# Optimization experiments

Hardware: AMD Instinct MI355X
Metric: run time of the kernel (lower is better)

Reference implementation:

```python
import jax, jax.numpy as jnp
import numpy as np

EMBED = 1024
MLP = 2048
N_EXPERTS = 8
TOP_K = 2


def setup_inputs() -> dict:
    key = jax.random.key(0)
    ks = jax.random.split(key, 5)
    scale_e = 1.0 / np.sqrt(EMBED)
    scale_m = 1.0 / np.sqrt(MLP)
    x = jax.random.normal(ks[0], (4, 2048, EMBED), dtype=jnp.float32)
    gate_w = jax.random.normal(ks[1], (EMBED, N_EXPERTS), dtype=jnp.float32) * scale_e
    w1 = jax.random.normal(ks[2], (N_EXPERTS, EMBED, MLP), dtype=jnp.float32) * scale_e
    w3 = jax.random.normal(ks[3], (N_EXPERTS, EMBED, MLP), dtype=jnp.float32) * scale_e
    w2 = jax.random.normal(ks[4], (N_EXPERTS, MLP, EMBED), dtype=jnp.float32) * scale_m
    return {"x": x, "gate_w": gate_w, "w1": w1, "w2": w2, "w3": w3}


def reference(x, gate_w, w1, w2, w3):
    B, S, D = x.shape
    xf = x.reshape(-1, D)  # [T, D] tokens
    # Router: softmax over experts, top-k select, renormalize selected weights
    router_logits = xf @ gate_w                      # [T, E]
    routing_weights = jax.nn.softmax(router_logits, axis=-1)
    sel_w, sel_e = jax.lax.top_k(routing_weights, TOP_K)  # [T, K]
    sel_w = sel_w / jnp.sum(sel_w, axis=-1, keepdims=True)
    out = jnp.zeros_like(xf)
    # Loop over the small fixed expert set; tokens not routed to expert e get
    # coefficient 0, matching the gather/scatter-add combine of the original.
    for e in range(N_EXPERTS):
        coef = jnp.sum(jnp.where(sel_e == e, sel_w, 0.0), axis=-1)  # [T]
        h = jax.nn.silu(xf @ w1[e]) * (xf @ w3[e])                  # [T, Mlp] SwiGLU
        out = out + coef[:, None] * (h @ w2[e])                     # [T, D]
    return out.reshape(B, S, D)
```

## Files before the change

kernel.cpp:

```cpp
#include <hip/hip_runtime.h>

#define EMBED 1024
#define MLP   2048
#define MLP2  4096
#define NE    8
#define NTOK  8192
#define RMAX  (2*NTOK + NE*256)

typedef _Float16 f16x8 __attribute__((ext_vector_type(8)));
typedef _Float16 f16x4 __attribute__((ext_vector_type(4)));
typedef float    f32x4 __attribute__((ext_vector_type(4)));

__device__ __forceinline__ void async_copy16(const void* g, void* l) {
  __builtin_amdgcn_global_load_lds(
      (const __attribute__((address_space(1))) unsigned int*)g,
      (__attribute__((address_space(3))) unsigned int*)l, 16, 0, 0);
}

__global__ __launch_bounds__(256) void router_kernel(
    const float* __restrict__ x, const float* __restrict__ gw,
    int* __restrict__ sel_e, float* __restrict__ sel_w, int* __restrict__ counts)
{
  __shared__ float gwt[NE * EMBED];
  __shared__ int cnt[NE];
  int tid = threadIdx.x;
  for (int idx = tid; idx < NE * EMBED; idx += 256) {
    int i = idx >> 3, e = idx & 7;
    gwt[e * EMBED + i] = gw[idx];
  }
  if (tid < NE) cnt[tid] = 0;
  __syncthreads();

  int lane = tid & 63, wv = tid >> 6;
  int t = blockIdx.x * 4 + wv;
  const float4* xr = (const float4*)(x + (size_t)t * EMBED);
  const float4* gt4 = (const float4*)gwt;
  float acc[NE];
  #pragma unroll
  for (int e = 0; e < NE; ++e) acc[e] = 0.f;
  #pragma unroll
  for (int c = 0; c < 4; ++c) {
    float4 xv = xr[c * 64 + lane];
    #pragma unroll
    for (int e = 0; e < NE; ++e) {
      float4 gv = gt4[e * 256 + c * 64 + lane];
      acc[e] += xv.x * gv.x + xv.y * gv.y + xv.z * gv.z + xv.w * gv.w;
    }
  }
  #pragma unroll
  for (int off = 1; off < 64; off <<= 1) {
    #pragma unroll
    for (int e = 0; e < NE; ++e) acc[e] += __shfl_xor(acc[e], off);
  }
  if (lane == 0) {
    int e0 = 0; float l0 = acc[0];
    #pragma unroll
    for (int e = 1; e < NE; ++e) if (acc[e] > l0) { l0 = acc[e]; e0 = e; }
    int e1 = -1; float l1 = -1e30f;
    #pragma unroll
    for (int e = 0; e < NE; ++e) if (e != e0 && acc[e] > l1) { l1 = acc[e]; e1 = e; }
    float w0 = 1.f / (1.f + expf(l1 - l0));
    sel_e[2 * t] = e0;     sel_w[2 * t] = w0;
    sel_e[2 * t + 1] = e1; sel_w[2 * t + 1] = 1.f - w0;
    atomicAdd(&cnt[e0], 1); atomicAdd(&cnt[e1], 1);
  }
  __syncthreads();
  if (tid < NE && cnt[tid]) atomicAdd(&counts[tid], cnt[tid]);
}

__global__ __launch_bounds__(256) void assign_kernel(
    const int* __restrict__ sel_e, const float* __restrict__ sel_w,
    const int* __restrict__ counts, int* __restrict__ cursor,
    int* __restrict__ offs_out, int* __restrict__ rowtok,
    float* __restrict__ rowcoef, int* __restrict__ inv)
{
  int offl[NE];
  {
    int o = 0;
    #pragma unroll
    for (int e = 0; e < NE; ++e) { offl[e] = o; o += (counts[e] + 255) & ~255; }
    if (blockIdx.x == 0 && threadIdx.x == 0) {
      #pragma unroll
      for (int e = 0; e < NE; ++e) offs_out[e] = offl[e];
      offs_out[NE] = o;
    }
  }
  int t = blockIdx.x * 256 + threadIdx.x;
  int lane = threadIdx.x & 63;
  #pragma unroll
  for (int k = 0; k < 2; ++k) {
    int e = sel_e[2 * t + k];
    float w = sel_w[2 * t + k];
    for (int xch = 0; xch < NE; ++xch) {
      unsigned long long m = __ballot(e == xch);
      if (e == xch) {
        int leader = __ffsll((unsigned long long)m) - 1;
        int base = 0;
        if (lane == leader) base = atomicAdd(&cursor[xch], (int)__popcll(m));
        base = __shfl(base, leader);
        int pos = offl[xch] + base + (int)__popcll(m & ((1ull << lane) - 1));
        rowtok[pos] = t;
        rowcoef[pos] = w;
        inv[2 * t + k] = pos;
      }
    }
  }
}

__global__ __launch_bounds__(256) void gather_kernel(
    const float* __restrict__ x, const int* __restrict__ rowtok,
    _Float16* __restrict__ xg)
{
  int r = blockIdx.x;
  int tok = rowtok[r];
  int t4 = threadIdx.x * 4;
  _Float16* dst = xg + (size_t)r * EMBED + t4;
  if (tok >= 0) {
    float4 v = *(const float4*)(x + (size_t)tok * EMBED + t4);
    f16x4 h; h.x = (_Float16)v.x; h.y = (_Float16)v.y; h.z = (_Float16)v.z; h.w = (_Float16)v.w;
    *(f16x4*)dst = h;
  } else {
    f16x4 z = {(_Float16)0.f, (_Float16)0.f, (_Float16)0.f, (_Float16)0.f};
    *(f16x4*)dst = z;
  }
}

__global__ __launch_bounds__(256) void transpose_all_kernel(
    const float* __restrict__ w1, const float* __restrict__ w3,
    const float* __restrict__ w2, _Float16* __restrict__ w13t,
    _Float16* __restrict__ w2t)
{
  int id = blockIdx.x;
  int mat = id >> 12;
  int rr = id & 4095;
  int e = rr >> 9, tile = rr & 511;
  const float* src; _Float16* dst; int K, N; size_t estride;
  if (mat == 0)      { src = w1; dst = w13t; K = EMBED; N = MLP; estride = (size_t)MLP2 * EMBED; }
  else if (mat == 1) { src = w3; dst = w13t; K = EMBED; N = MLP; estride = (size_t)MLP2 * EMBED; }
  else               { src = w2; dst = w2t;  K = MLP;   N = EMBED; estride = (size_t)MLP * EMBED; }
  int nx = K >> 6;
  int k0 = (tile % nx) * 64, n0 = (tile / nx) * 64;
  src += (size_t)e * K * N;
  dst += (size_t)e * estride;

  __shared__ float tilebuf[64][65];
  int t = threadIdx.x;
  int r = t >> 4, c4 = (t & 15) * 4;
  #pragma unroll
  for (int i = 0; i < 4; ++i) {
    float4 v = *(const float4*)(src + (size_t)(k0 + r + 16 * i) * N + n0 + c4);
    tilebuf[r + 16 * i][c4 + 0] = v.x;
    tilebuf[r + 16 * i][c4 + 1] = v.y;
    tilebuf[r + 16 * i][c4 + 2] = v.z;
    tilebuf[r + 16 * i][c4 + 3] = v.w;
  }
  __syncthreads();
  int kk8 = (t & 7) * 8, nIdx = t >> 3;
  #pragma unroll
  for (int i = 0; i < 2; ++i) {
    int n = nIdx + 32 * i;
    f16x8 h;
    #pragma unroll
    for (int j = 0; j < 8; ++j) h[j] = (_Float16)tilebuf[kk8 + j][n];
    int nn = n0 + n;
    size_t drow;
    if (mat == 2) drow = nn;
    else          drow = 2 * (nn & ~15) + (nn & 15) + (mat == 1 ? 16 : 0);
    *(f16x8*)(dst + drow * K + k0 + kk8) = h;
  }
}

__device__ __forceinline__ int resolve_expert(const int* __restrict__ offs, int r0)
{
  int e = 0;
  #pragma unroll
  for (int q = 0; q < NE - 1; ++q) if (r0 >= offs[q + 1]) e = q + 1;
  return e;
}

__device__ __forceinline__ void swz72(int& x, int& y)
{
  int lin = blockIdx.y * 72 + blockIdx.x;
  int xcd = lin & 7, idx = lin >> 3;
  x = xcd * 9 + idx % 9;
  y = idx / 9;
}


__global__ __launch_bounds__(512, 2) void gemm1_kernel(
    const _Float16* __restrict__ xg, const _Float16* __restrict__ w13t,
    const float* __restrict__ rowcoef, const int* __restrict__ offs,
    _Float16* __restrict__ hb)
{
  int bx, by; swz72(bx, by);
  int r0 = bx * 256;
  if (r0 >= offs[NE]) return;
  int e = resolve_expert(offs, r0);
  int n0 = by * 256;
  const _Float16* Bw = w13t + (size_t)e * MLP2 * EMBED;

  __shared__ __align__(16) _Float16 As[2][256 * 64];
  __shared__ __align__(16) _Float16 Bs[2][256 * 64];

  int tid = threadIdx.x, lane = tid & 63, wv = tid >> 6;
  int wm = (wv & 1) << 7;
  int wn = (wv >> 1) << 6;
  int l16 = lane & 15, quad = lane >> 4;

  int lc   = (lane & 7) ^ (lane >> 3);
  int loff = (lane >> 3) * EMBED + (lc << 3);
  int lrow = wv * 8;
  char* As0 = (char*)&As[0][0]; char* As1 = (char*)&As[1][0];
  char* Bs0 = (char*)&Bs[0][0]; char* Bs1 = (char*)&Bs[1][0];

  f32x4 acc[8][4];
  f32x4 z4 = {0.f, 0.f, 0.f, 0.f};
  #pragma unroll
  for (int i = 0; i < 8; ++i)
    #pragma unroll
    for (int j = 0; j < 4; ++j) acc[i][j] = z4;

  auto stageA = [&](char* dst, int kt, int o) {
    const _Float16* g = xg + (size_t)(r0 + o * 64 + lrow) * EMBED + kt * 64 + loff;
    async_copy16(g, dst + (o * 64 + lrow) * 128);
  };
  auto stageB = [&](char* dst, int kt, int o) {
    const _Float16* g = Bw + (size_t)(n0 + o * 64 + lrow) * EMBED + kt * 64 + loff;
    async_copy16(g, dst + (o * 64 + lrow) * 128);
  };
  auto frag = [&](const char* buf, int row, int clog) -> f16x8 {
    return *(const f16x8*)(buf + row * 128 + (((clog ^ (row & 7))) << 4));
  };

  const int NSTEP = EMBED / 64;
  #pragma unroll
  for (int o = 0; o < 4; ++o) { stageA(As0, 0, o); stageB(Bs0, 0, o); }

  char* Ac = As0; char* An = As1; char* Bc = Bs0; char* Bn = Bs1;
  for (int t = 0; t < NSTEP; ++t) {
    if (t + 1 < NSTEP) {
      #pragma unroll
      for (int o = 0; o < 4; ++o) stageA(An, t + 1, o);
      asm volatile("s_waitcnt vmcnt(4)" ::: "memory");
    } else {
      asm volatile("s_waitcnt vmcnt(0)" ::: "memory");
    }
    asm volatile("s_barrier" ::: "memory");

    f16x8 af[8], bf[4];
    #pragma unroll
    for (int i = 0; i < 8; ++i) af[i] = frag(Ac, wm + 16 * i + l16, quad);
    #pragma unroll
    for (int j = 0; j < 4; ++j) bf[j] = frag(Bc, wn + 16 * j + l16, quad);
    if (t + 1 < NSTEP) {
      #pragma unroll
      for (int o = 0; o < 4; ++o) stageB(Bn, t + 1, o);
    }
    __builtin_amdgcn_s_setprio(1);
    #pragma unroll
    for (int i = 0; i < 8; ++i)
      #pragma unroll
      for (int j = 0; j < 4; ++j)
        acc[i][j] = __builtin_amdgcn_mfma_f32_16x16x32_f16(af[i], bf[j], acc[i][j], 0, 0, 0);
    __builtin_amdgcn_s_setprio(0);
    #pragma unroll
    for (int i = 0; i < 8; ++i) af[i] = frag(Ac, wm + 16 * i + l16, 4 + quad);
    #pragma unroll
    for (int j = 0; j < 4; ++j) bf[j] = frag(Bc, wn + 16 * j + l16, 4 + quad);
    asm volatile("s_waitcnt lgkmcnt(0)" ::: "memory");
    asm volatile("s_barrier" ::: "memory");
    __builtin_amdgcn_s_setprio(1);
    #pragma unroll
    for (int i = 0; i < 8; ++i)
      #pragma unroll
      for (int j = 0; j < 4; ++j)
        acc[i][j] = __builtin_amdgcn_mfma_f32_16x16x32_f16(af[i], bf[j], acc[i][j], 0, 0, 0);
    __builtin_amdgcn_s_setprio(0);

    char* tmp;
    tmp = Ac; Ac = An; An = tmp;
    tmp = Bc; Bc = Bn; Bn = tmp;
  }

  int colbase = (((n0 + wn) >> 5) << 4) + l16;
  #pragma unroll
  for (int i = 0; i < 8; ++i) {
    int mb = r0 + wm + 16 * i + quad * 4;
    float cf[4];
    #pragma unroll
    for (int rg = 0; rg < 4; ++rg) cf[rg] = rowcoef[mb + rg];
    #pragma unroll
    for (int p = 0; p < 2; ++p) {
      int col = colbase + 16 * p;
      #pragma unroll
      for (int rg = 0; rg < 4; ++rg) {
        float g = acc[i][2 * p][rg], u = acc[i][2 * p + 1][rg];
        float h = g * u * cf[rg] / (1.f + __expf(-g));
        hb[(size_t)(mb + rg) * MLP + col] = (_Float16)h;
      }
    }
  }
}

__global__ __launch_bounds__(512, 2) void gemm2_kernel(
    const _Float16* __restrict__ hb, const _Float16* __restrict__ w2t,
    const int* __restrict__ offs, _Float16* __restrict__ hb2)
{
  int bx, by; swz72(bx, by);
  int r0 = bx * 256;
  if (r0 >= offs[NE]) return;
  int e = resolve_expert(offs, r0);
  int n0 = by * 256;
  const _Float16* Bw = w2t + (size_t)e * EMBED * MLP;

  __shared__ __align__(16) _Float16 As[2][256 * 64];
  __shared__ __align__(16) _Float16 Bs[2][256 * 64];

  int tid = threadIdx.x, lane = tid & 63, wv = tid >> 6;
  int wm = (wv & 1) << 7;
  int wn = (wv >> 1) << 6;
  int l16 = lane & 15, quad = lane >> 4;

  int lc   = (lane & 7) ^ (lane >> 3);
  int loff = (lane >> 3) * MLP + (lc << 3);
  int lrow = wv * 8;
  char* As0 = (char*)&As[0][0]; char* As1 = (char*)&As[1][0];
  char* Bs0 = (char*)&Bs[0][0]; char* Bs1 = (char*)&Bs[1][0];

  f32x4 acc[8][4];
  f32x4 z4 = {0.f, 0.f, 0.f, 0.f};
  #pragma unroll
  for (int i = 0; i < 8; ++i)
    #pragma unroll
    for (int j = 0; j < 4; ++j) acc[i][j] = z4;

  auto stageA = [&](char* dst, int kt, int o) {
    const _Float16* g = hb + (size_t)(r0 + o * 64 + lrow) * MLP + kt * 64 + loff;
    async_copy16(g, dst + (o * 64 + lrow) * 128);
  };
  auto stageB = [&](char* dst, int kt, int o) {
    const _Float16* g = Bw + (size_t)(n0 + o * 64 + lrow) * MLP + kt * 64 + loff;
    async_copy16(g, dst + (o * 64 + lrow) * 128);
  };
  auto frag = [&](const char* buf, int row, int clog) -> f16x8 {
    return *(const f16x8*)(buf + row * 128 + (((clog ^ (row & 7))) << 4));
  };

  const int NSTEP = MLP / 64;
  #pragma unroll
  for (int o = 0; o < 4; ++o) { stageA(As0, 0, o); stageB(Bs0, 0, o); }

  char* Ac = As0; char* An = As1; char* Bc = Bs0; char* Bn = Bs1;
  for (int t = 0; t < NSTEP; ++t) {
    if (t + 1 < NSTEP) {
      #pragma unroll
      for (int o = 0; o < 4; ++o) stageA(An, t + 1, o);
      asm volatile("s_waitcnt vmcnt(4)" ::: "memory");
    } else {
      asm volatile("s_waitcnt vmcnt(0)" ::: "memory");
    }
    asm volatile("s_barrier" ::: "memory");

    f16x8 af[8], bf[4];
    #pragma unroll
    for (int i = 0; i < 8; ++i) af[i] = frag(Ac, wm + 16 * i + l16, quad);
    #pragma unroll
    for (int j = 0; j < 4; ++j) bf[j] = frag(Bc, wn + 16 * j + l16, quad);
    if (t + 1 < NSTEP) {
      #pragma unroll
      for (int o = 0; o < 4; ++o) stageB(Bn, t + 1, o);
    }
    __builtin_amdgcn_s_setprio(1);
    #pragma unroll
    for (int i = 0; i < 8; ++i)
      #pragma unroll
      for (int j = 0; j < 4; ++j)
        acc[i][j] = __builtin_amdgcn_mfma_f32_16x16x32_f16(af[i], bf[j], acc[i][j], 0, 0, 0);
    __builtin_amdgcn_s_setprio(0);
    #pragma unroll
    for (int i = 0; i < 8; ++i) af[i] = frag(Ac, wm + 16 * i + l16, 4 + quad);
    #pragma unroll
    for (int j = 0; j < 4; ++j) bf[j] = frag(Bc, wn + 16 * j + l16, 4 + quad);
    asm volatile("s_waitcnt lgkmcnt(0)" ::: "memory");
    asm volatile("s_barrier" ::: "memory");
    __builtin_amdgcn_s_setprio(1);
    #pragma unroll
    for (int i = 0; i < 8; ++i)
      #pragma unroll
      for (int j = 0; j < 4; ++j)
        acc[i][j] = __builtin_amdgcn_mfma_f32_16x16x32_f16(af[i], bf[j], acc[i][j], 0, 0, 0);
    __builtin_amdgcn_s_setprio(0);

    char* tmp;
    tmp = Ac; Ac = An; An = tmp;
    tmp = Bc; Bc = Bn; Bn = tmp;
  }

  #pragma unroll
  for (int i = 0; i < 8; ++i) {
    int mb = r0 + wm + 16 * i + quad * 4;
    #pragma unroll
    for (int j = 0; j < 4; ++j) {
      int col = n0 + wn + 16 * j + l16;
      #pragma unroll
      for (int rg = 0; rg < 4; ++rg)
        hb2[(size_t)(mb + rg) * EMBED + col] = (_Float16)acc[i][j][rg];
    }
  }
}

__global__ __launch_bounds__(256) void combine_kernel(
    const _Float16* __restrict__ hb2, const int* __restrict__ inv,
    float* __restrict__ out)
{
  int t = blockIdx.x;
  int d = threadIdx.x * 4;
  int p0 = inv[2 * t], p1 = inv[2 * t + 1];
  f16x4 a = *(const f16x4*)(hb2 + (size_t)p0 * EMBED + d);
  f16x4 b = *(const f16x4*)(hb2 + (size_t)p1 * EMBED + d);
  float4 r;
  r.x = (float)a.x + (float)b.x;
  r.y = (float)a.y + (float)b.y;
  r.z = (float)a.z + (float)b.z;
  r.w = (float)a.w + (float)b.w;
  *(float4*)(out + (size_t)t * EMBED + d) = r;
}

extern "C" void kernel_launch(void* const* d_in, const int* in_sizes, int n_in,
                              void* d_out, int out_size, void* d_ws, size_t ws_size,
                              hipStream_t stream)
{
  (void)in_sizes; (void)n_in; (void)ws_size; (void)out_size;
  const float* x  = (const float*)d_in[0];
  const float* gw = (const float*)d_in[1];
  const float* w1 = (const float*)d_in[2];
  const float* w2 = (const float*)d_in[3];
  const float* w3 = (const float*)d_in[4];
  float* out = (float*)d_out;
  char* ws = (char*)d_ws;

  size_t o = 0;
  auto alloc = [&](size_t bytes) { size_t r = o; o = (o + bytes + 255) & ~255ULL; return r; };
  _Float16* w13t = (_Float16*)(ws + alloc((size_t)NE * MLP2 * EMBED * 2));
  _Float16* w2t  = (_Float16*)(ws + alloc((size_t)NE * MLP * EMBED * 2));
  _Float16* xg   = (_Float16*)(ws + alloc((size_t)RMAX * EMBED * 2));
  _Float16* hb   = (_Float16*)(ws + alloc((size_t)RMAX * MLP * 2));
  int*   rowtok  = (int*)(ws + alloc((size_t)RMAX * 4));
  float* rowcoef = (float*)(ws + alloc((size_t)RMAX * 4));
  int*   sel_e   = (int*)(ws + alloc((size_t)2 * NTOK * 4));
  float* sel_w   = (float*)(ws + alloc((size_t)2 * NTOK * 4));
  int*   inv     = (int*)(ws + alloc((size_t)2 * NTOK * 4));
  int*   meta    = (int*)(ws + alloc(256));
  int* counts = meta;
  int* offs   = meta + 8;
  int* cursor = meta + 17;
  _Float16* hb2 = xg;

  hipMemsetAsync(meta, 0, 256, stream);
  hipMemsetAsync(rowtok, 0xFF, (size_t)RMAX * 4, stream);
  hipMemsetAsync(rowcoef, 0, (size_t)RMAX * 4, stream);

  transpose_all_kernel<<<3 * 4096, 256, 0, stream>>>(w1, w3, w2, w13t, w2t);

  router_kernel<<<NTOK / 4, 256, 0, stream>>>(x, gw, sel_e, sel_w, counts);
  assign_kernel<<<NTOK / 256, 256, 0, stream>>>(sel_e, sel_w, counts, cursor,
                                                offs, rowtok, rowcoef, inv);
  gather_kernel<<<RMAX, 256, 0, stream>>>(x, rowtok, xg);

  gemm1_kernel<<<dim3(RMAX / 256, MLP2 / 256), 512, 0, stream>>>(xg, w13t, rowcoef, offs, hb);
  gemm2_kernel<<<dim3(RMAX / 256, EMBED / 256), 512, 0, stream>>>(hb, w2t, offs, hb2);
  combine_kernel<<<NTOK, 256, 0, stream>>>(hb2, inv, out);
}
```

Baseline: 588.9 us.

## Interleave LDS fragment loads, global prefetch and MFMA in four quadrant phases

Both grouped GEMM main loops now split each K-step into four sub-tile phases (A-low/B-low, A-low/B-high, A-high/B-high, A-high/B-low). Global-to-LDS prefetches for the next tile and fragment reads for the next phase are spread between the MFMA bursts, with extra barriers between phases. The aim is finer-grained overlap of memory traffic with matrix-core work and fewer live fragment registers at any one time. In exchange it adds several barriers per K-step, and the tighter vmcnt(2) wait could stall if loads arrive late.

```diff
diff --git a/kernel.cpp b/kernel.cpp
--- a/kernel.cpp
+++ b/kernel.cpp
@@ -238,44 +238,84 @@
 
   char* Ac = As0; char* An = As1; char* Bc = Bs0; char* Bn = Bs1;
   for (int t = 0; t < NSTEP; ++t) {
-    if (t + 1 < NSTEP) {
-      #pragma unroll
-      for (int o = 0; o < 4; ++o) stageA(An, t + 1, o);
-      asm volatile("s_waitcnt vmcnt(4)" ::: "memory");
+    bool pf = (t + 1 < NSTEP);
+    f16x8 afL[8], afH[8], bfA[4], bfB[4];
+    if (pf) {
+      stageA(An, t + 1, 0); stageA(An, t + 1, 1);
+      asm volatile("s_waitcnt vmcnt(2)" ::: "memory");
     } else {
       asm volatile("s_waitcnt vmcnt(0)" ::: "memory");
     }
     asm volatile("s_barrier" ::: "memory");
-
-    f16x8 af[8], bf[4];
-    #pragma unroll
-    for (int i = 0; i < 8; ++i) af[i] = frag(Ac, wm + 16 * i + l16, quad);
-    #pragma unroll
-    for (int j = 0; j < 4; ++j) bf[j] = frag(Bc, wn + 16 * j + l16, quad);
-    if (t + 1 < NSTEP) {
-      #pragma unroll
-      for (int o = 0; o < 4; ++o) stageB(Bn, t + 1, o);
-    }
-    __builtin_amdgcn_s_setprio(1);
-    #pragma unroll
-    for (int i = 0; i < 8; ++i)
-      #pragma unroll
-      for (int j = 0; j < 4; ++j)
-        acc[i][j] = __builtin_amdgcn_mfma_f32_16x16x32_f16(af[i], bf[j], acc[i][j], 0, 0, 0);
-    __builtin_amdgcn_s_setprio(0);
-    #pragma unroll
-    for (int i = 0; i < 8; ++i) af[i] = frag(Ac, wm + 16 * i + l16, 4 + quad);
-    #pragma unroll
-    for (int j = 0; j < 4; ++j) bf[j] = frag(Bc, wn + 16 * j + l16, 4 + quad);
+    #pragma unroll
+    for (int i = 0; i < 4; ++i) {
+      afL[2 * i]     = frag(Ac, wm + 16 * i + l16, quad);
+      afL[2 * i + 1] = frag(Ac, wm + 16 * i + l16, 4 + quad);
+    }
+    #pragma unroll
+    for (int j = 0; j < 2; ++j) {
+      bfA[2 * j]     = frag(Bc, wn + 16 * j + l16, quad);
+      bfA[2 * j + 1] = frag(Bc, wn + 16 * j + l16, 4 + quad);
+    }
     asm volatile("s_waitcnt lgkmcnt(0)" ::: "memory");
-    asm volatile("s_barrier" ::: "memory");
-    __builtin_amdgcn_s_setprio(1);
-    #pragma unroll
-    for (int i = 0; i < 8; ++i)
-      #pragma unroll
-      for (int j = 0; j < 4; ++j)
-        acc[i][j] = __builtin_amdgcn_mfma_f32_16x16x32_f16(af[i], bf[j], acc[i][j], 0, 0, 0);
-    __builtin_amdgcn_s_setprio(0);
+    __builtin_amdgcn_s_setprio(1);
+    #pragma unroll
+    for (int i = 0; i < 4; ++i)
+      #pragma unroll
+      for (int j = 0; j < 2; ++j) {
+        acc[i][j] = __builtin_amdgcn_mfma_f32_16x16x32_f16(afL[2 * i], bfA[2 * j], acc[i][j], 0, 0, 0);
+        acc[i][j] = __builtin_amdgcn_mfma_f32_16x16x32_f16(afL[2 * i + 1], bfA[2 * j + 1], acc[i][j], 0, 0, 0);
+      }
+    __builtin_amdgcn_s_setprio(0);
+    asm volatile("s_barrier" ::: "memory");
+    if (pf) { stageA(An, t + 1, 2); stageA(An, t + 1, 3); }
+    #pragma unroll
+    for (int j = 0; j < 2; ++j) {
+      bfB[2 * j]     = frag(Bc, wn + 16 * (j + 2) + l16, quad);
+      bfB[2 * j + 1] = frag(Bc, wn + 16 * (j + 2) + l16, 4 + quad);
+    }
+    asm volatile("s_barrier" ::: "memory");
+    asm volatile("s_waitcnt lgkmcnt(0)" ::: "memory");
+    __builtin_amdgcn_s_setprio(1);
+    #pragma unroll
+    for (int i = 0; i < 4; ++i)
+      #pragma unroll
+      for (int j = 0; j < 2; ++j) {
+        acc[i][j + 2] = __builtin_amdgcn_mfma_f32_16x16x32_f16(afL[2 * i], bfB[2 * j], acc[i][j + 2], 0, 0, 0);
+        acc[i][j + 2] = __builtin_amdgcn_mfma_f32_16x16x32_f16(afL[2 * i + 1], bfB[2 * j + 1], acc[i][j + 2], 0, 0, 0);
+      }
+    __builtin_amdgcn_s_setprio(0);
+    asm volatile("s_barrier" ::: "memory");
+    if (pf) { stageB(Bn, t + 1, 0); stageB(Bn, t + 1, 1); }
+    #pragma unroll
+    for (int i = 0; i < 4; ++i) {
+      afH[2 * i]     = frag(Ac, wm + 16 * (i + 4) + l16, quad);
+      afH[2 * i + 1] = frag(Ac, wm + 16 * (i + 4) + l16, 4 + quad);
+    }
+    asm volatile("s_barrier" ::: "memory");
+    asm volatile("s_waitcnt lgkmcnt(0)" ::: "memory");
+    __builtin_amdgcn_s_setprio(1);
+    #pragma unroll
+    for (int i = 0; i < 4; ++i)
+      #pragma unroll
+      for (int j = 0; j < 2; ++j) {
+        acc[i + 4][j + 2] = __builtin_amdgcn_mfma_f32_16x16x32_f16(afH[2 * i], bfB[2 * j], acc[i + 4][j + 2], 0, 0, 0);
+        acc[i + 4][j + 2] = __builtin_amdgcn_mfma_f32_16x16x32_f16(afH[2 * i + 1], bfB[2 * j + 1], acc[i + 4][j + 2], 0, 0, 0);
+      }
+    __builtin_amdgcn_s_setprio(0);
+    asm volatile("s_barrier" ::: "memory");
+    if (pf) { stageB(Bn, t + 1, 2); stageB(Bn, t + 1, 3); }
+    asm volatile("s_barrier" ::: "memory");
+    __builtin_amdgcn_s_setprio(1);
+    #pragma unroll
+    for (int i = 0; i < 4; ++i)
+      #pragma unroll
+      for (int j = 0; j < 2; ++j) {
+        acc[i + 4][j] = __builtin_amdgcn_mfma_f32_16x16x32_f16(afH[2 * i], bfA[2 * j], acc[i + 4][j], 0, 0, 0);
+        acc[i + 4][j] = __builtin_amdgcn_mfma_f32_16x16x32_f16(afH[2 * i + 1], bfA[2 * j + 1], acc[i + 4][j], 0, 0, 0);
+      }
+    __builtin_amdgcn_s_setprio(0);
+    asm volatile("s_barrier" ::: "memory");
 
     char* tmp;
     tmp = Ac; Ac = An; An = tmp;
@@ -352,44 +392,84 @@
 
   char* Ac = As0; char* An = As1; char* Bc = Bs0; char* Bn = Bs1;
   for (int t = 0; t < NSTEP; ++t) {
-    if (t + 1 < NSTEP) {
-      #pragma unroll
-      for (int o = 0; o < 4; ++o) stageA(An, t + 1, o);
-      asm volatile("s_waitcnt vmcnt(4)" ::: "memory");
+    bool pf = (t + 1 < NSTEP);
+    f16x8 afL[8], afH[8], bfA[4], bfB[4];
+    if (pf) {
+      stageA(An, t + 1, 0); stageA(An, t + 1, 1);
+      asm volatile("s_waitcnt vmcnt(2)" ::: "memory");
     } else {
       asm volatile("s_waitcnt vmcnt(0)" ::: "memory");
     }
     asm volatile("s_barrier" ::: "memory");
-
-    f16x8 af[8], bf[4];
-    #pragma unroll
-    for (int i = 0; i < 8; ++i) af[i] = frag(Ac, wm + 16 * i + l16, quad);
-    #pragma unroll
-    for (int j = 0; j < 4; ++j) bf[j] = frag(Bc, wn + 16 * j + l16, quad);
-    if (t + 1 < NSTEP) {
-      #pragma unroll
-      for (int o = 0; o < 4; ++o) stageB(Bn, t + 1, o);
-    }
-    __builtin_amdgcn_s_setprio(1);
-    #pragma unroll
-    for (int i = 0; i < 8; ++i)
-      #pragma unroll
-      for (int j = 0; j < 4; ++j)
-        acc[i][j] = __builtin_amdgcn_mfma_f32_16x16x32_f16(af[i], bf[j], acc[i][j], 0, 0, 0);
-    __builtin_amdgcn_s_setprio(0);
-    #pragma unroll
-    for (int i = 0; i < 8; ++i) af[i] = frag(Ac, wm + 16 * i + l16, 4 + quad);
-    #pragma unroll
-    for (int j = 0; j < 4; ++j) bf[j] = frag(Bc, wn + 16 * j + l16, 4 + quad);
+    #pragma unroll
+    for (int i = 0; i < 4; ++i) {
+      afL[2 * i]     = frag(Ac, wm + 16 * i + l16, quad);
+      afL[2 * i + 1] = frag(Ac, wm + 16 * i + l16, 4 + quad);
+    }
+    #pragma unroll
+    for (int j = 0; j < 2; ++j) {
+      bfA[2 * j]     = frag(Bc, wn + 16 * j + l16, quad);
+      bfA[2 * j + 1] = frag(Bc, wn + 16 * j + l16, 4 + quad);
+    }
     asm volatile("s_waitcnt lgkmcnt(0)" ::: "memory");
-    asm volatile("s_barrier" ::: "memory");
-    __builtin_amdgcn_s_setprio(1);
-    #pragma unroll
-    for (int i = 0; i < 8; ++i)
-      #pragma unroll
-      for (int j = 0; j < 4; ++j)
-        acc[i][j] = __builtin_amdgcn_mfma_f32_16x16x32_f16(af[i], bf[j], acc[i][j], 0, 0, 0);
-    __builtin_amdgcn_s_setprio(0);
+    __builtin_amdgcn_s_setprio(1);
+    #pragma unroll
+    for (int i = 0; i < 4; ++i)
+      #pragma unroll
+      for (int j = 0; j < 2; ++j) {
+        acc[i][j] = __builtin_amdgcn_mfma_f32_16x16x32_f16(afL[2 * i], bfA[2 * j], acc[i][j], 0, 0, 0);
+        acc[i][j] = __builtin_amdgcn_mfma_f32_16x16x32_f16(afL[2 * i + 1], bfA[2 * j + 1], acc[i][j], 0, 0, 0);
+      }
+    __builtin_amdgcn_s_setprio(0);
+    asm volatile("s_barrier" ::: "memory");
+    if (pf) { stageA(An, t + 1, 2); stageA(An, t + 1, 3); }
+    #pragma unroll
+    for (int j = 0; j < 2; ++j) {
+      bfB[2 * j]     = frag(Bc, wn + 16 * (j + 2) + l16, quad);
+      bfB[2 * j + 1] = frag(Bc, wn + 16 * (j + 2) + l16, 4 + quad);
+    }
+    asm volatile("s_barrier" ::: "memory");
+    asm volatile("s_waitcnt lgkmcnt(0)" ::: "memory");
+    __builtin_amdgcn_s_setprio(1);
+    #pragma unroll
+    for (int i = 0; i < 4; ++i)
+      #pragma unroll
+      for (int j = 0; j < 2; ++j) {
+        acc[i][j + 2] = __builtin_amdgcn_mfma_f32_16x16x32_f16(afL[2 * i], bfB[2 * j], acc[i][j + 2], 0, 0, 0);
+        acc[i][j + 2] = __builtin_amdgcn_mfma_f32_16x16x32_f16(afL[2 * i + 1], bfB[2 * j + 1], acc[i][j + 2], 0, 0, 0);
+      }
+    __builtin_amdgcn_s_setprio(0);
+    asm volatile("s_barrier" ::: "memory");
+    if (pf) { stageB(Bn, t + 1, 0); stageB(Bn, t + 1, 1); }
+    #pragma unroll
+    for (int i = 0; i < 4; ++i) {
+      afH[2 * i]     = frag(Ac, wm + 16 * (i + 4) + l16, quad);
+      afH[2 * i + 1] = frag(Ac, wm + 16 * (i + 4) + l16, 4 + quad);
+    }
+    asm volatile("s_barrier" ::: "memory");
+    asm volatile("s_waitcnt lgkmcnt(0)" ::: "memory");
+    __builtin_amdgcn_s_setprio(1);
+    #pragma unroll
+    for (int i = 0; i < 4; ++i)
+      #pragma unroll
+      for (int j = 0; j < 2; ++j) {
+        acc[i + 4][j + 2] = __builtin_amdgcn_mfma_f32_16x16x32_f16(afH[2 * i], bfB[2 * j], acc[i + 4][j + 2], 0, 0, 0);
+        acc[i + 4][j + 2] = __builtin_amdgcn_mfma_f32_16x16x32_f16(afH[2 * i + 1], bfB[2 * j + 1], acc[i + 4][j + 2], 0, 0, 0);
+      }
+    __builtin_amdgcn_s_setprio(0);
+    asm volatile("s_barrier" ::: "memory");
+    if (pf) { stageB(Bn, t + 1, 2); stageB(Bn, t + 1, 3); }
+    asm volatile("s_barrier" ::: "memory");
+    __builtin_amdgcn_s_setprio(1);
+    #pragma unroll
+    for (int i = 0; i < 4; ++i)
+      #pragma unroll
+      for (int j = 0; j < 2; ++j) {
+        acc[i + 4][j] = __builtin_amdgcn_mfma_f32_16x16x32_f16(afH[2 * i], bfA[2 * j], acc[i + 4][j], 0, 0, 0);
+        acc[i + 4][j] = __builtin_amdgcn_mfma_f32_16x16x32_f16(afH[2 * i + 1], bfA[2 * j + 1], acc[i + 4][j], 0, 0, 0);
+      }
+    __builtin_amdgcn_s_setprio(0);
+    asm volatile("s_barrier" ::: "memory");
 
     char* tmp;
     tmp = Ac; Ac = An; An = tmp;
```

Measured after the change: 621.3 us. 1.05x slower.
